# Kernel tuning notes

Hardware: AMD Instinct MI355X
Metric: run time of the kernel (lower is better)

The kernel has to match this reference:

```python
import jax, jax.numpy as jnp
import numpy as np

N_USERS, N_ITEMS, EMB_DIM, N_INTENTS, N_EDGES, N_LAYERS = 50000, 100000, 64, 128, 3000000, 2
N_NODES = N_USERS + N_ITEMS


def _l2norm(x, eps=1e-8):
    # F.normalize(p=2, dim=-1, eps): x / max(||x||, eps)
    n = jnp.sqrt(jnp.sum(x * x, axis=-1, keepdims=True))
    return x / jnp.maximum(n, eps)


def setup_inputs() -> dict:
    key = jax.random.key(0)
    k0, k1, k2, k3, k4, k5 = jax.random.split(key, 6)
    xav_e = np.sqrt(2.0 / (N_NODES + EMB_DIM)).astype(np.float32)
    xav_i = np.sqrt(2.0 / (EMB_DIM + N_INTENTS)).astype(np.float32)
    return {
        "user_emb": jax.random.normal(k0, (N_USERS, EMB_DIM), jnp.float32) * xav_e,
        "item_emb": jax.random.normal(k1, (N_ITEMS, EMB_DIM), jnp.float32) * xav_e,
        "user_intent": jax.random.normal(k2, (EMB_DIM, N_INTENTS), jnp.float32) * xav_i,
        "item_intent": jax.random.normal(k3, (EMB_DIM, N_INTENTS), jnp.float32) * xav_i,
        "all_h": jax.random.randint(k4, (N_EDGES,), 0, N_NODES, jnp.int32),
        "all_t": jax.random.randint(k5, (N_EDGES,), 0, N_NODES, jnp.int32),
    }


def reference(user_emb, item_emb, user_intent, item_intent, all_h, all_t):
    E = all_h.shape[0]

    def spmm(vals, x):
        # y[h] += vals * x[t]  over edges  (torch_sparse.spmm)
        return jax.ops.segment_sum(vals[:, None] * x[all_t], all_h, num_segments=N_NODES)

    # _cal_sparse_adj: G = D^-1/2 A D^-1/2 on the unweighted edge list
    deg = jax.ops.segment_sum(jnp.ones((E,), jnp.float32), all_h, num_segments=N_NODES)
    d_inv_sqrt = jnp.where(deg > 0, deg, 1.0) ** -0.5 * (deg > 0)
    g_values = d_inv_sqrt[all_h] * d_inv_sqrt[all_t]

    def adaptive_values(src):
        # _adaptive_mask: cosine-sim edge weights, row-normalized
        he = _l2norm(src[all_h])
        te = _l2norm(src[all_t])
        edge_alpha = (jnp.sum(he * te, axis=1) + 1.0) * 0.5  # in [0,1]
        row_sum = jax.ops.segment_sum(edge_alpha, all_h, num_segments=N_NODES)
        d_inv = jnp.where(row_sum > 0, 1.0 / jnp.where(row_sum > 0, row_sum, 1.0), 0.0)
        return d_inv[all_h] * edge_alpha

    emb = jnp.concatenate([user_emb, item_emb], axis=0)  # [N, d]
    acc = emb
    for _ in range(N_LAYERS):
        gnn = spmm(g_values, emb)
        u, it = emb[:N_USERS], emb[N_USERS:]
        u_int = jax.nn.softmax(u @ user_intent, axis=1) @ user_intent.T
        i_int = jax.nn.softmax(it @ item_intent, axis=1) @ item_intent.T
        int_e = jnp.concatenate([u_int, i_int], axis=0)
        gaa = spmm(adaptive_values(gnn), emb)
        iaa = spmm(adaptive_values(int_e), emb)
        emb = gnn + int_e + gaa + iaa + emb
        acc = acc + emb
    # torch: sum over stacked layer embeddings == initial + each layer output
    return acc
```

## Files before the change

kernel.cpp:

```cpp
#include <hip/hip_runtime.h>
#include <hip/hip_bf16.h>

#define N_USERS   50000
#define N_ITEMS   100000
#define N_NODES   150000
#define DIM       64
#define N_INTENTS 128
#define N_EDGES   3000000
#define PSHIFT    9
#define PROWS     (1 << PSHIFT)
#define NPART     ((N_NODES + PROWS - 1) >> PSHIFT)
#define CHUNK     16384
#define NCHB      ((N_EDGES + CHUNK - 1) / CHUNK)
#define RECB      256

#define UT_TILES  (N_USERS / 16)
#define TOT_TILES ((N_USERS + N_ITEMS) / 16)
#define INT_B     ((TOT_TILES + 3) / 4)

typedef __attribute__((ext_vector_type(8))) short short8v;
typedef __attribute__((ext_vector_type(4))) float f32x4;
typedef __attribute__((ext_vector_type(2))) float f32x2;

template<int CTRL>
static __device__ __forceinline__ float dpp_ror_add(float x){
  int t = __builtin_amdgcn_update_dpp(0, __builtin_bit_cast(int, x),
                                      CTRL, 0xF, 0xF, true);
  return x + __builtin_bit_cast(float, t);
}
static __device__ __forceinline__ float row16_allsum(float x){
  x = dpp_ror_add<0x128>(x);
  x = dpp_ror_add<0x124>(x);
  x = dpp_ror_add<0x122>(x);
  x = dpp_ror_add<0x121>(x);
  return x;
}
template<int CTRL>
static __device__ __forceinline__ float dpp_ror_max(float x){
  int t = __builtin_amdgcn_update_dpp(0, __builtin_bit_cast(int, x),
                                      CTRL, 0xF, 0xF, true);
  return fmaxf(x, __builtin_bit_cast(float, t));
}
static __device__ __forceinline__ float row16_allmax(float x){
  x = dpp_ror_max<0x128>(x);
  x = dpp_ror_max<0x124>(x);
  x = dpp_ror_max<0x122>(x);
  x = dpp_ror_max<0x121>(x);
  return x;
}

static __device__ __forceinline__ unsigned short f2bf(float x){
  __hip_bfloat16 h = __float2bfloat16(x);
  return __builtin_bit_cast(unsigned short, h);
}
static __device__ __forceinline__ float bf_lo(unsigned int v){
  return __builtin_bit_cast(float, v << 16);
}
static __device__ __forceinline__ float bf_hi(unsigned int v){
  return __builtin_bit_cast(float, v & 0xFFFF0000u);
}
static __device__ __forceinline__ float bfval(unsigned short h){
  return __builtin_bit_cast(float, (unsigned int)h << 16);
}
static __device__ __forceinline__ void split2(float x, unsigned short& hi,
                                              unsigned short& lo){
  hi = f2bf(x);
  lo = f2bf(x - bfval(hi));
}

static __device__ __forceinline__ void fp8dec8(uint2 v, float* f){
  f32x2 a = __builtin_amdgcn_cvt_pk_f32_fp8(v.x, false);
  f32x2 b = __builtin_amdgcn_cvt_pk_f32_fp8(v.x, true);
  f32x2 c = __builtin_amdgcn_cvt_pk_f32_fp8(v.y, false);
  f32x2 d = __builtin_amdgcn_cvt_pk_f32_fp8(v.y, true);
  f[0]=a[0]; f[1]=a[1]; f[2]=b[0]; f[3]=b[1];
  f[4]=c[0]; f[5]=c[1]; f[6]=d[0]; f[7]=d[1];
}
static __device__ __forceinline__ unsigned int fp8pack4(float a, float b,
                                                        float c, float d){
  unsigned int v = __builtin_amdgcn_cvt_pk_fp8_f32(a, b, 0, false);
  return __builtin_amdgcn_cvt_pk_fp8_f32(c, d, v, true);
}
static __device__ __forceinline__ unsigned char f2fp8(float x){
  return (unsigned char)(__builtin_amdgcn_cvt_pk_fp8_f32(x, x, 0, false) & 0xFF);
}

__global__ void k_init(const float* __restrict__ ue, const float* __restrict__ ie,
                       float* __restrict__ emb, float* __restrict__ acc){
  int i = blockIdx.x * 256 + threadIdx.x;
  if (i >= N_NODES * DIM) return;
  float v = (i < N_USERS * DIM) ? ue[i] : ie[i - N_USERS * DIM];
  emb[i] = v; acc[i] = v;
}

__global__ void k_embd0(const float* __restrict__ emb, const float* __restrict__ dis,
                        uint2* __restrict__ embd2, unsigned char* __restrict__ rec0){
  int i = blockIdx.x * 256 + threadIdx.x;
  if (i >= N_NODES * 16) return;
  int n = i >> 4, sub = i & 15;
  float d = dis[n];
  float4 v = ((const float4*)emb)[i];
  uint2 ob;
  ob.x = (unsigned)f2bf(d * v.x) | ((unsigned)f2bf(d * v.y) << 16);
  ob.y = (unsigned)f2bf(d * v.z) | ((unsigned)f2bf(d * v.w) << 16);
  embd2[i] = ob;
  uint2 eb;
  eb.x = (unsigned)f2bf(v.x) | ((unsigned)f2bf(v.y) << 16);
  eb.y = (unsigned)f2bf(v.z) | ((unsigned)f2bf(v.w) << 16);
  *(uint2*)(rec0 + (size_t)n * RECB + 128 + 8 * sub) = eb;
}

__global__ void k_deg(const int* __restrict__ h, int* __restrict__ deg){
  int e = blockIdx.x * 256 + threadIdx.x;
  if (e < N_EDGES) atomicAdd(&deg[h[e]], 1);
}

__global__ void k_scan1(const int* __restrict__ deg, int* __restrict__ tmp,
                        int* __restrict__ aux){
  __shared__ int s[256];
  int t = threadIdx.x, i = blockIdx.x * 256 + t;
  int v = (i < N_NODES) ? deg[i] : 0;
  s[t] = v; __syncthreads();
  for (int off = 1; off < 256; off <<= 1){
    int x = (t >= off) ? s[t - off] : 0;
    __syncthreads();
    s[t] += x;
    __syncthreads();
  }
  if (i < N_NODES) tmp[i] = s[t];
  if (t == 255) aux[blockIdx.x] = s[255];
}

__global__ __launch_bounds__(1024) void k_scan2(int* __restrict__ aux, int n){
  __shared__ int s[1024];
  int t = threadIdx.x;
  int v = (t < n) ? aux[t] : 0;
  s[t] = v; __syncthreads();
  for (int off = 1; off < 1024; off <<= 1){
    int x = (t >= off) ? s[t - off] : 0;
    __syncthreads();
    s[t] += x;
    __syncthreads();
  }
  if (t < n) aux[t] = s[t] - v;
}

__global__ void k_rowptr(const int* __restrict__ tmp, const int* __restrict__ deg,
                         const int* __restrict__ aux, int* __restrict__ rp,
                         float* __restrict__ dis, int* __restrict__ gcur){
  int i = blockIdx.x * 256 + threadIdx.x;
  if (i < N_NODES){
    int v = aux[i >> 8] + tmp[i] - deg[i];
    rp[i] = v;
    int d = deg[i];
    dis[i] = (d > 0) ? (1.f / sqrtf((float)d)) : 0.f;
    if ((i & (PROWS - 1)) == 0) gcur[i >> PSHIFT] = v;
  }
  if (i == 0) rp[N_NODES] = N_EDGES;
}

__global__ __launch_bounds__(256) void k_part1(const int* __restrict__ h,
                                               const int* __restrict__ t,
                                               int* __restrict__ gcur,
                                               unsigned int* __restrict__ stg){
  __shared__ int hist[NPART];
  __shared__ int base[NPART];
  __shared__ int cnt2[NPART];
  int tid = threadIdx.x;
  int s = blockIdx.x * CHUNK;
  int e = min(s + CHUNK, N_EDGES);
  for (int p = tid; p < NPART; p += 256){ hist[p] = 0; cnt2[p] = 0; }
  __syncthreads();
  for (int i = s + tid; i < e; i += 256)
    atomicAdd(&hist[h[i] >> PSHIFT], 1);
  __syncthreads();
  for (int p = tid; p < NPART; p += 256){
    int c = hist[p];
    base[p] = c ? atomicAdd(&gcur[p], c) : 0;
  }
  __syncthreads();
  for (int i = s + tid; i < e; i += 256){
    int hh = h[i];
    int part = hh >> PSHIFT;
    int pos = base[part] + atomicAdd(&cnt2[part], 1);
    stg[pos] = ((unsigned)t[i] << PSHIFT) | (unsigned)(hh & (PROWS - 1));
  }
}

__global__ __launch_bounds__(256) void k_part2(const int* __restrict__ rp,
                                               const unsigned int* __restrict__ stg,
                                               int* __restrict__ t_csr){
  __shared__ int cur[PROWS];
  int b = blockIdx.x, tid = threadIdx.x;
  int row0 = b << PSHIFT;
  int rows = min(PROWS, N_NODES - row0);
  for (int i = tid; i < rows; i += 256) cur[i] = rp[row0 + i];
  __syncthreads();
  int s = rp[row0], e = rp[row0 + rows];
  for (int i = s + tid; i < e; i += 256){
    unsigned int v = stg[i];
    int pos = atomicAdd(&cur[v & (PROWS - 1)], 1);
    t_csr[pos] = (int)(v >> PSHIFT);
  }
}

__global__ void k_spmm_gnn(const int* __restrict__ rp, const int* __restrict__ t_csr,
                           const float* __restrict__ dis,
                           const unsigned short* __restrict__ embd,
                           float* __restrict__ gnn, unsigned char* __restrict__ rec){
  int w = (blockIdx.x * 256 + threadIdx.x) >> 6;
  int lane = threadIdx.x & 63;
  if (w >= N_NODES) return;
  int slot = lane >> 3, sub = lane & 7;
  int s = rp[w], e = rp[w + 1];
  float a0=0.f,a1=0.f,a2=0.f,a3=0.f,a4=0.f,a5=0.f,a6=0.f,a7=0.f;
  for (int i = s + slot; i < e; i += 8){
    int t = t_csr[i];
    uint4 ev = *(const uint4*)(embd + (size_t)t * 64 + 8 * sub);
    a0 += bf_lo(ev.x); a1 += bf_hi(ev.x);
    a2 += bf_lo(ev.y); a3 += bf_hi(ev.y);
    a4 += bf_lo(ev.z); a5 += bf_hi(ev.z);
    a6 += bf_lo(ev.w); a7 += bf_hi(ev.w);
  }
#pragma unroll
  for (int m = 8; m <= 32; m <<= 1){
    a0 += __shfl_xor(a0, m, 64); a1 += __shfl_xor(a1, m, 64);
    a2 += __shfl_xor(a2, m, 64); a3 += __shfl_xor(a3, m, 64);
    a4 += __shfl_xor(a4, m, 64); a5 += __shfl_xor(a5, m, 64);
    a6 += __shfl_xor(a6, m, 64); a7 += __shfl_xor(a7, m, 64);
  }
  float dw = dis[w];
  float g0 = dw*a0, g1 = dw*a1, g2 = dw*a2, g3 = dw*a3;
  float g4 = dw*a4, g5 = dw*a5, g6 = dw*a6, g7 = dw*a7;
  float sq = g0*g0 + g1*g1 + g2*g2 + g3*g3 + g4*g4 + g5*g5 + g6*g6 + g7*g7;
#pragma unroll
  for (int m = 1; m <= 4; m <<= 1) sq += __shfl_xor(sq, m, 64);
  float invn = 1.f / fmaxf(sqrtf(sq), 1e-8f);
  if (slot == 0){
    float4 v0 = make_float4(g0, g1, g2, g3);
    float4 v1 = make_float4(g4, g5, g6, g7);
    ((float4*)gnn)[w * 16 + 2 * sub]     = v0;
    ((float4*)gnn)[w * 16 + 2 * sub + 1] = v1;
    uint2 o;
    o.x = fp8pack4(g0*invn, g1*invn, g2*invn, g3*invn);
    o.y = fp8pack4(g4*invn, g5*invn, g6*invn, g7*invn);
    *(uint2*)(rec + (size_t)w * RECB + 8 * sub) = o;
  }
}

__global__ void k_wprep(const float* __restrict__ wu, const float* __restrict__ wi,
                        unsigned short* __restrict__ wbuf){
  const float* W = blockIdx.x ? wi : wu;
  unsigned short* seg = wbuf + blockIdx.x * 32768;
  int tid = threadIdx.x;
  for (int i = tid; i < DIM * N_INTENTS; i += 256){
    unsigned short h, l; split2(W[i], h, l);
    seg[16384 + i] = h; seg[24576 + i] = l;
  }
  for (int idx = tid; idx < 16 * 64; idx += 256){
    int f = idx >> 6, lane = idx & 63;
    int nt = f >> 1, ks = f & 1, g = lane >> 4, c = lane & 15;
    int in = 16 * nt + c;
#pragma unroll
    for (int e = 0; e < 8; e++){
      int d = 8 * g + e + 32 * ks;
      unsigned short h, l; split2(W[d * N_INTENTS + in], h, l);
      seg[f * 512 + lane * 8 + e] = h;
      seg[8192 + f * 512 + lane * 8 + e] = l;
    }
  }
}

__global__ __launch_bounds__(256) void k_intent_mfma(
    const unsigned short* __restrict__ wbuf, const float* __restrict__ emb,
    unsigned short* __restrict__ out_bf, unsigned char* __restrict__ rec){
  __shared__ __align__(16) unsigned int Pl[4][2048];
  int wid = threadIdx.x >> 6, lane = threadIdx.x & 63;
  int tile = blockIdx.x * 4 + wid;
  if (tile >= TOT_TILES) return;
  int node0; const unsigned short* wseg;
  if (tile < UT_TILES){ node0 = tile * 16;                         wseg = wbuf; }
  else                { node0 = N_USERS + (tile - UT_TILES) * 16;  wseg = wbuf + 32768; }
  int g = lane >> 4, c = lane & 15;

  const float4* erow = (const float4*)(emb + (size_t)(node0 + c) * DIM);
  float4 ea0 = erow[2 * g],     eb0 = erow[2 * g + 1];
  float4 ea1 = erow[8 + 2 * g], eb1 = erow[9 + 2 * g];
  short8v ehi[2], elo[2];
  {
    float xs[16] = {ea0.x, ea0.y, ea0.z, ea0.w, eb0.x, eb0.y, eb0.z, eb0.w,
                    ea1.x, ea1.y, ea1.z, ea1.w, eb1.x, eb1.y, eb1.z, eb1.w};
#pragma unroll
    for (int ksi = 0; ksi < 2; ksi++)
#pragma unroll
      for (int e = 0; e < 8; e++){
        unsigned short h, l; split2(xs[ksi * 8 + e], h, l);
        ehi[ksi][e] = (short)h; elo[ksi][e] = (short)l;
      }
  }

  const uint4* w1hi = (const uint4*)wseg;
  const uint4* w1lo = (const uint4*)(wseg + 8192);
  f32x4 acc1[8];
#pragma unroll
  for (int nt = 0; nt < 8; nt++){
    f32x4 a = {0.f, 0.f, 0.f, 0.f};
#pragma unroll
    for (int ks = 0; ks < 2; ks++){
      short8v wh = __builtin_bit_cast(short8v, w1hi[(nt * 2 + ks) * 64 + lane]);
      short8v wl = __builtin_bit_cast(short8v, w1lo[(nt * 2 + ks) * 64 + lane]);
      a = __builtin_amdgcn_mfma_f32_16x16x32_bf16(ehi[ks], wh, a, 0, 0, 0);
      a = __builtin_amdgcn_mfma_f32_16x16x32_bf16(elo[ks], wh, a, 0, 0, 0);
      a = __builtin_amdgcn_mfma_f32_16x16x32_bf16(ehi[ks], wl, a, 0, 0, 0);
    }
    acc1[nt] = a;
  }

  unsigned int* pw = &Pl[wid][0];
#pragma unroll
  for (int r = 0; r < 4; r++){
    float m = acc1[0][r];
#pragma unroll
    for (int nt = 1; nt < 8; nt++) m = fmaxf(m, acc1[nt][r]);
    m = row16_allmax(m);
    float p[8];
    float s = 0.f;
#pragma unroll
    for (int nt = 0; nt < 8; nt++){ p[nt] = __expf(acc1[nt][r] - m); s += p[nt]; }
    s = row16_allsum(s);
    float inv = 1.f / s;
    int node = 4 * g + r;
    int swz = (node & 7) << 2;
    int base = node * 128 + c;
#pragma unroll
    for (int nt = 0; nt < 8; nt++){
      float v = p[nt] * inv;
      unsigned short h, l; split2(v, h, l);
      pw[(base + 16 * nt) ^ swz] = (unsigned int)h | ((unsigned int)l << 16);
    }
  }

  const uint4* pr = (const uint4*)pw;
  short8v phf[4], plf[4];
  int sw = (c & 7) << 2;
#pragma unroll
  for (int ks = 0; ks < 4; ks++){
    int i0 = c * 128 + 8 * g + 32 * ks;
    uint4 ra = pr[(i0 ^ sw) >> 2];
    uint4 rb = pr[((i0 + 4) ^ sw) >> 2];
    unsigned int q[8] = {ra.x, ra.y, ra.z, ra.w, rb.x, rb.y, rb.z, rb.w};
#pragma unroll
    for (int e = 0; e < 8; e++){
      phf[ks][e] = (short)(q[e] & 0xFFFFu);
      plf[ks][e] = (short)(q[e] >> 16);
    }
  }

  const uint4* w2hi = (const uint4*)(wseg + 16384);
  const uint4* w2lo = (const uint4*)(wseg + 24576);
  f32x4 acc2[4];
#pragma unroll
  for (int nt = 0; nt < 4; nt++){
    f32x4 a = {0.f, 0.f, 0.f, 0.f};
#pragma unroll
    for (int ks = 0; ks < 4; ks++){
      int fi = (16 * nt + c) * 16 + ks * 4 + g;
      short8v wh = __builtin_bit_cast(short8v, w2hi[fi]);
      short8v wl = __builtin_bit_cast(short8v, w2lo[fi]);
      a = __builtin_amdgcn_mfma_f32_16x16x32_bf16(phf[ks], wh, a, 0, 0, 0);
      a = __builtin_amdgcn_mfma_f32_16x16x32_bf16(plf[ks], wh, a, 0, 0, 0);
      a = __builtin_amdgcn_mfma_f32_16x16x32_bf16(phf[ks], wl, a, 0, 0, 0);
    }
    acc2[nt] = a;
  }

#pragma unroll
  for (int r = 0; r < 4; r++){
    float sq = 0.f;
#pragma unroll
    for (int nt = 0; nt < 4; nt++) sq = fmaf(acc2[nt][r], acc2[nt][r], sq);
    sq = row16_allsum(sq);
    float invn = 1.f / fmaxf(sqrtf(sq), 1e-8f);
    size_t node = (size_t)(node0 + 4 * g + r);
    unsigned char* hw = rec + node * RECB + 64;
    size_t obase = node * DIM + c;
#pragma unroll
    for (int nt = 0; nt < 4; nt++){
      float v = acc2[nt][r];
      out_bf[obase + 16 * nt] = f2bf(v);
      hw[16 * nt + c] = f2fp8(v * invn);
    }
  }
}

__global__ void k_adafuse(const int* __restrict__ rp, const int* __restrict__ t_csr,
                          const unsigned char* __restrict__ rec,
                          const uint2* __restrict__ inte_bf2,
                          const float* __restrict__ emb,
                          const float* __restrict__ dis,
                          float* __restrict__ gnn_io, float* __restrict__ acc,
                          uint2* __restrict__ embd_next2,
                          unsigned char* __restrict__ rec_next,
                          int write_next){
  int w = (blockIdx.x * 256 + threadIdx.x) >> 6;
  int lane = threadIdx.x & 63;
  if (w >= N_NODES) return;
  int slot = lane >> 4, sub = lane & 15;
  const unsigned char* wrec = rec + (size_t)w * RECB;
  float wv[8];
  fp8dec8(*(const uint2*)(wrec + 8 * sub), wv);
  bool isA = sub < 8;
  int s = rp[w], e = rp[w + 1];
  float4 s1 = make_float4(0.f, 0.f, 0.f, 0.f);
  float4 s2 = make_float4(0.f, 0.f, 0.f, 0.f);
  float r1 = 0.f, r2 = 0.f;
  for (int i = s + slot; i < e; i += 4){
    int t = t_csr[i];
    const unsigned char* tr = rec + (size_t)t * RECB;
    float tv[8];
    fp8dec8(*(const uint2*)(tr + 8 * sub), tv);
    float part = wv[0]*tv[0] + wv[1]*tv[1] + wv[2]*tv[2] + wv[3]*tv[3]
               + wv[4]*tv[4] + wv[5]*tv[5] + wv[6]*tv[6] + wv[7]*tv[7];
    part += __shfl_xor(part, 1, 64);
    part += __shfl_xor(part, 2, 64);
    part += __shfl_xor(part, 4, 64);
    float other = __shfl_xor(part, 8, 64);
    float p = isA ? part : other;
    float q = isA ? other : part;
    float a1 = fmaf(p, 0.5f, 0.5f);
    float a2 = fmaf(q, 0.5f, 0.5f);
    r1 += a1; r2 += a2;
    uint2 ev = *(const uint2*)(tr + 128 + 8 * sub);
    float v0 = bf_lo(ev.x), v1 = bf_hi(ev.x), v2 = bf_lo(ev.y), v3 = bf_hi(ev.y);
    s1.x = fmaf(a1, v0, s1.x); s1.y = fmaf(a1, v1, s1.y);
    s1.z = fmaf(a1, v2, s1.z); s1.w = fmaf(a1, v3, s1.w);
    s2.x = fmaf(a2, v0, s2.x); s2.y = fmaf(a2, v1, s2.y);
    s2.z = fmaf(a2, v2, s2.z); s2.w = fmaf(a2, v3, s2.w);
  }
#pragma unroll
  for (int m = 16; m <= 32; m <<= 1){
    s1.x += __shfl_xor(s1.x, m, 64); s1.y += __shfl_xor(s1.y, m, 64);
    s1.z += __shfl_xor(s1.z, m, 64); s1.w += __shfl_xor(s1.w, m, 64);
    s2.x += __shfl_xor(s2.x, m, 64); s2.y += __shfl_xor(s2.y, m, 64);
    s2.z += __shfl_xor(s2.z, m, 64); s2.w += __shfl_xor(s2.w, m, 64);
    r1   += __shfl_xor(r1,   m, 64); r2   += __shfl_xor(r2,   m, 64);
  }
  float d1 = (r1 > 0.f) ? 1.f / r1 : 0.f;
  float d2 = (r2 > 0.f) ? 1.f / r2 : 0.f;
  if (slot == 0){
    int idx4 = w * 16 + sub;
    float4 gg = ((float4*)gnn_io)[idx4];
    uint2 it = inte_bf2[idx4];
    float4 em = ((const float4*)emb)[idx4];
    float4 nv;
    nv.x = gg.x + bf_lo(it.x) + em.x + d1 * s1.x + d2 * s2.x;
    nv.y = gg.y + bf_hi(it.x) + em.y + d1 * s1.y + d2 * s2.y;
    nv.z = gg.z + bf_lo(it.y) + em.z + d1 * s1.z + d2 * s2.z;
    nv.w = gg.w + bf_hi(it.y) + em.w + d1 * s1.w + d2 * s2.w;
    ((float4*)gnn_io)[idx4] = nv;
    float4 ac = ((float4*)acc)[idx4];
    ac.x += nv.x; ac.y += nv.y; ac.z += nv.z; ac.w += nv.w;
    ((float4*)acc)[idx4] = ac;
    if (write_next){
      float dw = dis[w];
      uint2 od;
      od.x = (unsigned)f2bf(dw * nv.x) | ((unsigned)f2bf(dw * nv.y) << 16);
      od.y = (unsigned)f2bf(dw * nv.z) | ((unsigned)f2bf(dw * nv.w) << 16);
      embd_next2[idx4] = od;
      uint2 ob;
      ob.x = (unsigned)f2bf(nv.x) | ((unsigned)f2bf(nv.y) << 16);
      ob.y = (unsigned)f2bf(nv.z) | ((unsigned)f2bf(nv.w) << 16);
      *(uint2*)(rec_next + (size_t)w * RECB + 128 + 8 * sub) = ob;
    }
  }
}

extern "C" void kernel_launch(void* const* d_in, const int* in_sizes, int n_in,
                              void* d_out, int out_size, void* d_ws, size_t ws_size,
                              hipStream_t stream){
  const float* ue = (const float*)d_in[0];
  const float* ie = (const float*)d_in[1];
  const float* wu = (const float*)d_in[2];
  const float* wi = (const float*)d_in[3];
  const int* all_h = (const int*)d_in[4];
  const int* all_t = (const int*)d_in[5];
  float* acc = (float*)d_out;

  char* p = (char*)d_ws;
  auto take = [&](size_t bytes)->char*{
    char* r = p; p += (bytes + 255) & ~size_t(255); return r;
  };
  float*  embA  = (float*)take(sizeof(float) * N_NODES * DIM);
  float*  embB  = (float*)take(sizeof(float) * N_NODES * DIM);
  unsigned char* rec0 = (unsigned char*)take((size_t)N_NODES * RECB);
  unsigned char* rec1 = (unsigned char*)take((size_t)N_NODES * RECB);
  unsigned short* inte_bf = (unsigned short*)take(sizeof(short) * N_NODES * DIM);
  unsigned short* embd    = (unsigned short*)take(sizeof(short) * N_NODES * DIM);
  unsigned short* wbuf    = (unsigned short*)take(sizeof(short) * 2 * 32768);
  int*    t_csr = (int*)take(sizeof(int) * N_EDGES);
  float*  dis   = (float*)take(sizeof(float) * N_NODES);
  int*    deg   = (int*)take(sizeof(int) * N_NODES);
  int*    tmp   = (int*)take(sizeof(int) * N_NODES);
  int*    aux   = (int*)take(sizeof(int) * 1024);
  int*    rp    = (int*)take(sizeof(int) * (N_NODES + 1));
  int*    gcur  = (int*)take(sizeof(int) * NPART);
  if ((size_t)(p - (char*)d_ws) > ws_size) return;
  unsigned int* stg = (unsigned int*)rec1;

  const int ELEM_B  = (N_NODES * DIM + 255) / 256;
  const int ELEM4_B = (N_NODES * 16 + 255) / 256;
  const int NODEW_B = (N_NODES * 64 + 255) / 256;
  const int EDGE_B  = (N_EDGES + 255) / 256;
  const int NODE_B  = (N_NODES + 255) / 256;

  hipMemsetAsync(deg, 0, sizeof(int) * N_NODES, stream);
  k_init<<<ELEM_B, 256, 0, stream>>>(ue, ie, embA, acc);
  k_wprep<<<2, 256, 0, stream>>>(wu, wi, wbuf);
  k_deg<<<EDGE_B, 256, 0, stream>>>(all_h, deg);
  k_scan1<<<NODE_B, 256, 0, stream>>>(deg, tmp, aux);
  k_scan2<<<1, 1024, 0, stream>>>(aux, NODE_B);
  k_rowptr<<<NODE_B, 256, 0, stream>>>(tmp, deg, aux, rp, dis, gcur);
  k_embd0<<<ELEM4_B, 256, 0, stream>>>(embA, dis, (uint2*)embd, rec0);
  k_part1<<<NCHB, 256, 0, stream>>>(all_h, all_t, gcur, stg);
  k_part2<<<NPART, 256, 0, stream>>>(rp, stg, t_csr);

  float* eA = embA;
  float* eB = embB;
  unsigned char* recC = rec0;
  unsigned char* recN = rec1;
  for (int layer = 0; layer < 2; layer++){
    k_spmm_gnn<<<NODEW_B, 256, 0, stream>>>(rp, t_csr, dis, embd, eB, recC);
    k_intent_mfma<<<INT_B, 256, 0, stream>>>(wbuf, eA, inte_bf, recC);
    k_adafuse<<<NODEW_B, 256, 0, stream>>>(rp, t_csr, recC,
                                           (const uint2*)inte_bf,
                                           eA, dis, eB, acc,
                                           (uint2*)embd, recN,
                                           layer == 0 ? 1 : 0);
    float* t = eA; eA = eB; eB = t;
    unsigned char* tr = recC; recC = recN; recN = tr;
  }
}
```

Measured before the change: 937.9 us.

## Software-pipeline SpMM gathers and widen adafuse to 8 edges per wave

k_spmm_gnn now prefetches the next column index and the next embedding row (a two-stage software pipeline), so gather latency overlaps the accumulation. k_adafuse is remapped from 4 edge slots × 16 lanes to 8 slots × 8 lanes, with 16-byte fp8 and bf16 loads per lane, which doubles the edges processed in parallel per wave. The gnn_io store is skipped on the last layer, where it is not consumed. In exchange each adafuse lane holds more registers, which may lower occupancy, and the prefetch adds clamped redundant index loads.

```diff
diff --git a/kernel.cpp b/kernel.cpp
--- a/kernel.cpp
+++ b/kernel.cpp
@@ -75,6 +75,10 @@
   f32x2 d = __builtin_amdgcn_cvt_pk_f32_fp8(v.y, true);
   f[0]=a[0]; f[1]=a[1]; f[2]=b[0]; f[3]=b[1];
   f[4]=c[0]; f[5]=c[1]; f[6]=d[0]; f[7]=d[1];
+}
+static __device__ __forceinline__ void fp8dec16(uint4 v, float* f){
+  fp8dec8(make_uint2(v.x, v.y), f);
+  fp8dec8(make_uint2(v.z, v.w), f + 8);
 }
 static __device__ __forceinline__ unsigned int fp8pack4(float a, float b,
                                                         float c, float d){
@@ -214,13 +218,20 @@
   int slot = lane >> 3, sub = lane & 7;
   int s = rp[w], e = rp[w + 1];
   float a0=0.f,a1=0.f,a2=0.f,a3=0.f,a4=0.f,a5=0.f,a6=0.f,a7=0.f;
-  for (int i = s + slot; i < e; i += 8){
-    int t = t_csr[i];
-    uint4 ev = *(const uint4*)(embd + (size_t)t * 64 + 8 * sub);
-    a0 += bf_lo(ev.x); a1 += bf_hi(ev.x);
-    a2 += bf_lo(ev.y); a3 += bf_hi(ev.y);
-    a4 += bf_lo(ev.z); a5 += bf_hi(ev.z);
-    a6 += bf_lo(ev.w); a7 += bf_hi(ev.w);
+  if (e > s){
+    int i = s + slot;
+    int t0 = t_csr[min(i, e - 1)];
+    int t1 = t_csr[min(i + 8, e - 1)];
+    uint4 ev0 = *(const uint4*)(embd + (size_t)t0 * 64 + 8 * sub);
+    for (; i < e; i += 8){
+      int t2 = t_csr[min(i + 16, e - 1)];
+      uint4 ev1 = *(const uint4*)(embd + (size_t)t1 * 64 + 8 * sub);
+      a0 += bf_lo(ev0.x); a1 += bf_hi(ev0.x);
+      a2 += bf_lo(ev0.y); a3 += bf_hi(ev0.y);
+      a4 += bf_lo(ev0.z); a5 += bf_hi(ev0.z);
+      a6 += bf_lo(ev0.w); a7 += bf_hi(ev0.w);
+      ev0 = ev1; t1 = t2;
+    }
   }
 #pragma unroll
   for (int m = 8; m <= 32; m <<= 1){
@@ -395,7 +406,7 @@
 
 __global__ void k_adafuse(const int* __restrict__ rp, const int* __restrict__ t_csr,
                           const unsigned char* __restrict__ rec,
-                          const uint2* __restrict__ inte_bf2,
+                          const unsigned short* __restrict__ inte_bf,
                           const float* __restrict__ emb,
                           const float* __restrict__ dis,
                           float* __restrict__ gnn_io, float* __restrict__ acc,
@@ -405,72 +416,93 @@
   int w = (blockIdx.x * 256 + threadIdx.x) >> 6;
   int lane = threadIdx.x & 63;
   if (w >= N_NODES) return;
-  int slot = lane >> 4, sub = lane & 15;
+  int slot = lane >> 3, sub = lane & 7;
   const unsigned char* wrec = rec + (size_t)w * RECB;
-  float wv[8];
-  fp8dec8(*(const uint2*)(wrec + 8 * sub), wv);
-  bool isA = sub < 8;
+  float wv[16];
+  fp8dec16(*(const uint4*)(wrec + 16 * sub), wv);
+  bool isA = sub < 4;
   int s = rp[w], e = rp[w + 1];
-  float4 s1 = make_float4(0.f, 0.f, 0.f, 0.f);
-  float4 s2 = make_float4(0.f, 0.f, 0.f, 0.f);
+  float s1[8] = {0.f,0.f,0.f,0.f,0.f,0.f,0.f,0.f};
+  float s2[8] = {0.f,0.f,0.f,0.f,0.f,0.f,0.f,0.f};
   float r1 = 0.f, r2 = 0.f;
-  for (int i = s + slot; i < e; i += 4){
+  for (int i = s + slot; i < e; i += 8){
     int t = t_csr[i];
     const unsigned char* tr = rec + (size_t)t * RECB;
-    float tv[8];
-    fp8dec8(*(const uint2*)(tr + 8 * sub), tv);
-    float part = wv[0]*tv[0] + wv[1]*tv[1] + wv[2]*tv[2] + wv[3]*tv[3]
-               + wv[4]*tv[4] + wv[5]*tv[5] + wv[6]*tv[6] + wv[7]*tv[7];
+    float tv[16];
+    fp8dec16(*(const uint4*)(tr + 16 * sub), tv);
+    float part = 0.f;
+#pragma unroll
+    for (int j = 0; j < 16; j++) part = fmaf(wv[j], tv[j], part);
     part += __shfl_xor(part, 1, 64);
     part += __shfl_xor(part, 2, 64);
-    part += __shfl_xor(part, 4, 64);
-    float other = __shfl_xor(part, 8, 64);
-    float p = isA ? part : other;
-    float q = isA ? other : part;
-    float a1 = fmaf(p, 0.5f, 0.5f);
-    float a2 = fmaf(q, 0.5f, 0.5f);
+    float other = __shfl_xor(part, 4, 64);
+    float pA = isA ? part : other;
+    float pB = isA ? other : part;
+    float a1 = fmaf(pA, 0.5f, 0.5f);
+    float a2 = fmaf(pB, 0.5f, 0.5f);
     r1 += a1; r2 += a2;
-    uint2 ev = *(const uint2*)(tr + 128 + 8 * sub);
+    uint4 ev = *(const uint4*)(tr + 128 + 16 * sub);
     float v0 = bf_lo(ev.x), v1 = bf_hi(ev.x), v2 = bf_lo(ev.y), v3 = bf_hi(ev.y);
-    s1.x = fmaf(a1, v0, s1.x); s1.y = fmaf(a1, v1, s1.y);
-    s1.z = fmaf(a1, v2, s1.z); s1.w = fmaf(a1, v3, s1.w);
-    s2.x = fmaf(a2, v0, s2.x); s2.y = fmaf(a2, v1, s2.y);
-    s2.z = fmaf(a2, v2, s2.z); s2.w = fmaf(a2, v3, s2.w);
-  }
-#pragma unroll
-  for (int m = 16; m <= 32; m <<= 1){
-    s1.x += __shfl_xor(s1.x, m, 64); s1.y += __shfl_xor(s1.y, m, 64);
-    s1.z += __shfl_xor(s1.z, m, 64); s1.w += __shfl_xor(s1.w, m, 64);
-    s2.x += __shfl_xor(s2.x, m, 64); s2.y += __shfl_xor(s2.y, m, 64);
-    s2.z += __shfl_xor(s2.z, m, 64); s2.w += __shfl_xor(s2.w, m, 64);
-    r1   += __shfl_xor(r1,   m, 64); r2   += __shfl_xor(r2,   m, 64);
+    float v4 = bf_lo(ev.z), v5 = bf_hi(ev.z), v6 = bf_lo(ev.w), v7 = bf_hi(ev.w);
+    s1[0] = fmaf(a1, v0, s1[0]); s1[1] = fmaf(a1, v1, s1[1]);
+    s1[2] = fmaf(a1, v2, s1[2]); s1[3] = fmaf(a1, v3, s1[3]);
+    s1[4] = fmaf(a1, v4, s1[4]); s1[5] = fmaf(a1, v5, s1[5]);
+    s1[6] = fmaf(a1, v6, s1[6]); s1[7] = fmaf(a1, v7, s1[7]);
+    s2[0] = fmaf(a2, v0, s2[0]); s2[1] = fmaf(a2, v1, s2[1]);
+    s2[2] = fmaf(a2, v2, s2[2]); s2[3] = fmaf(a2, v3, s2[3]);
+    s2[4] = fmaf(a2, v4, s2[4]); s2[5] = fmaf(a2, v5, s2[5]);
+    s2[6] = fmaf(a2, v6, s2[6]); s2[7] = fmaf(a2, v7, s2[7]);
+  }
+#pragma unroll
+  for (int m = 8; m <= 32; m <<= 1){
+#pragma unroll
+    for (int j = 0; j < 8; j++){
+      s1[j] += __shfl_xor(s1[j], m, 64);
+      s2[j] += __shfl_xor(s2[j], m, 64);
+    }
+    r1 += __shfl_xor(r1, m, 64);
+    r2 += __shfl_xor(r2, m, 64);
   }
   float d1 = (r1 > 0.f) ? 1.f / r1 : 0.f;
   float d2 = (r2 > 0.f) ? 1.f / r2 : 0.f;
   if (slot == 0){
-    int idx4 = w * 16 + sub;
-    float4 gg = ((float4*)gnn_io)[idx4];
-    uint2 it = inte_bf2[idx4];
-    float4 em = ((const float4*)emb)[idx4];
-    float4 nv;
-    nv.x = gg.x + bf_lo(it.x) + em.x + d1 * s1.x + d2 * s2.x;
-    nv.y = gg.y + bf_hi(it.x) + em.y + d1 * s1.y + d2 * s2.y;
-    nv.z = gg.z + bf_lo(it.y) + em.z + d1 * s1.z + d2 * s2.z;
-    nv.w = gg.w + bf_hi(it.y) + em.w + d1 * s1.w + d2 * s2.w;
-    ((float4*)gnn_io)[idx4] = nv;
-    float4 ac = ((float4*)acc)[idx4];
-    ac.x += nv.x; ac.y += nv.y; ac.z += nv.z; ac.w += nv.w;
-    ((float4*)acc)[idx4] = ac;
+    int ia = w * 16 + 2 * sub, ib = ia + 1;
+    float4 g0 = ((float4*)gnn_io)[ia];
+    float4 g1 = ((float4*)gnn_io)[ib];
+    uint4 it = *(const uint4*)(inte_bf + (size_t)w * 64 + 8 * sub);
+    float4 e0 = ((const float4*)emb)[ia];
+    float4 e1 = ((const float4*)emb)[ib];
+    float4 n0, n1;
+    n0.x = g0.x + bf_lo(it.x) + e0.x + d1 * s1[0] + d2 * s2[0];
+    n0.y = g0.y + bf_hi(it.x) + e0.y + d1 * s1[1] + d2 * s2[1];
+    n0.z = g0.z + bf_lo(it.y) + e0.z + d1 * s1[2] + d2 * s2[2];
+    n0.w = g0.w + bf_hi(it.y) + e0.w + d1 * s1[3] + d2 * s2[3];
+    n1.x = g1.x + bf_lo(it.z) + e1.x + d1 * s1[4] + d2 * s2[4];
+    n1.y = g1.y + bf_hi(it.z) + e1.y + d1 * s1[5] + d2 * s2[5];
+    n1.z = g1.z + bf_lo(it.w) + e1.z + d1 * s1[6] + d2 * s2[6];
+    n1.w = g1.w + bf_hi(it.w) + e1.w + d1 * s1[7] + d2 * s2[7];
+    float4 a0 = ((float4*)acc)[ia];
+    float4 a1v = ((float4*)acc)[ib];
+    a0.x += n0.x; a0.y += n0.y; a0.z += n0.z; a0.w += n0.w;
+    a1v.x += n1.x; a1v.y += n1.y; a1v.z += n1.z; a1v.w += n1.w;
+    ((float4*)acc)[ia] = a0;
+    ((float4*)acc)[ib] = a1v;
     if (write_next){
+      ((float4*)gnn_io)[ia] = n0;
+      ((float4*)gnn_io)[ib] = n1;
       float dw = dis[w];
-      uint2 od;
-      od.x = (unsigned)f2bf(dw * nv.x) | ((unsigned)f2bf(dw * nv.y) << 16);
-      od.y = (unsigned)f2bf(dw * nv.z) | ((unsigned)f2bf(dw * nv.w) << 16);
-      embd_next2[idx4] = od;
-      uint2 ob;
-      ob.x = (unsigned)f2bf(nv.x) | ((unsigned)f2bf(nv.y) << 16);
-      ob.y = (unsigned)f2bf(nv.z) | ((unsigned)f2bf(nv.w) << 16);
-      *(uint2*)(rec_next + (size_t)w * RECB + 128 + 8 * sub) = ob;
+      uint4 od;
+      od.x = (unsigned)f2bf(dw * n0.x) | ((unsigned)f2bf(dw * n0.y) << 16);
+      od.y = (unsigned)f2bf(dw * n0.z) | ((unsigned)f2bf(dw * n0.w) << 16);
+      od.z = (unsigned)f2bf(dw * n1.x) | ((unsigned)f2bf(dw * n1.y) << 16);
+      od.w = (unsigned)f2bf(dw * n1.z) | ((unsigned)f2bf(dw * n1.w) << 16);
+      *(uint4*)(embd_next2 + (size_t)w * 16 + 2 * sub) = od;
+      uint4 ob;
+      ob.x = (unsigned)f2bf(n0.x) | ((unsigned)f2bf(n0.y) << 16);
+      ob.y = (unsigned)f2bf(n0.z) | ((unsigned)f2bf(n0.w) << 16);
+      ob.z = (unsigned)f2bf(n1.x) | ((unsigned)f2bf(n1.y) << 16);
+      ob.w = (unsigned)f2bf(n1.z) | ((unsigned)f2bf(n1.w) << 16);
+      *(uint4*)(rec_next + (size_t)w * RECB + 128 + 16 * sub) = ob;
     }
   }
 }
@@ -531,8 +563,7 @@
   for (int layer = 0; layer < 2; layer++){
     k_spmm_gnn<<<NODEW_B, 256, 0, stream>>>(rp, t_csr, dis, embd, eB, recC);
     k_intent_mfma<<<INT_B, 256, 0, stream>>>(wbuf, eA, inte_bf, recC);
-    k_adafuse<<<NODEW_B, 256, 0, stream>>>(rp, t_csr, recC,
-                                           (const uint2*)inte_bf,
+    k_adafuse<<<NODEW_B, 256, 0, stream>>>(rp, t_csr, recC, inte_bf,
                                            eA, dis, eB, acc,
                                            (uint2*)embd, recN,
                                            layer == 0 ? 1 : 0);
```

After: 972.5 us. 1.04x slower.
